# Kernel tuning notes

Hardware: AMD Instinct MI355X
Metric: run time of the kernel (lower is better)

Reference implementation:

```python
import jax, jax.numpy as jnp
import numpy as np

EPS = 1e-8


def _three_nn_interpolate(coords, ref_coords, features):
    # coords: [B, N, 3], ref_coords: [B, M, 3], features: [B, C, M]
    # squared pairwise distances [B, N, M]
    d2 = (
        jnp.sum(coords * coords, axis=-1, keepdims=True)          # [B, N, 1]
        + jnp.sum(ref_coords * ref_coords, axis=-1)[:, None, :]    # [B, 1, M]
        - 2.0 * jnp.einsum('bnd,bmd->bnm', coords, ref_coords)
    )
    neg_d, idx = jax.lax.top_k(-d2, 3)       # 3 nearest -> idx [B, N, 3]
    dist = -neg_d                             # squared dists of 3-NN
    w = 1.0 / (dist + EPS)
    w = w / jnp.sum(w, axis=-1, keepdims=True)  # [B, N, 3]
    feats_t = jnp.swapaxes(features, 1, 2)    # [B, M, C]
    gathered = jax.vmap(lambda f, i: f[i])(feats_t, idx)  # [B, N, 3, C]
    out = jnp.einsum('bnk,bnkc->bcn', w, gathered)         # [B, C, N]
    return out


def setup_inputs() -> dict:
    key = jax.random.key(0)
    ks = jax.random.split(key, 5)
    B, N, M = 2, 16384, 4096
    return {
        'coords': jax.random.normal(ks[0], (B, N, 3), dtype=jnp.float32),
        'ref_coords': jax.random.normal(ks[1], (B, M, 3), dtype=jnp.float32),
        'ref_features': jax.random.normal(ks[2], (B, 256, M), dtype=jnp.float32),
        'ref_t_embed': jax.random.normal(ks[3], (B, 128, M), dtype=jnp.float32),
        'points_features': jax.random.normal(ks[4], (B, 64, N), dtype=jnp.float32),
    }


def reference(coords, ref_coords, ref_features, ref_t_embed, points_features):
    # PointNetFPModule.forward: interpolate features and t_embed from the
    # coarse ref point set onto the dense point set, then concat skip features.
    features = _three_nn_interpolate(coords, ref_coords, ref_features)  # [B, 256, N]
    t_embed = _three_nn_interpolate(coords, ref_coords, ref_t_embed)    # [B, 128, N]
    features = jnp.concatenate([features, points_features], axis=1)     # [B, 320, N]
    return features, t_embed
```

## Files before the change

### kernel.cpp

```cpp
#include <hip/hip_runtime.h>
#include <cstdint>

#define BB 2
#define NN 16384
#define MM 4096
#define CF 256
#define CT 128
#define CP 64

#define TPB1 512
#define NPB1 64
#define CHUNK 2048

__global__ __launch_bounds__(TPB1, 4) void knn_kernel(
    const float* __restrict__ coords,
    const float* __restrict__ ref_coords,
    int4* __restrict__ wsI,
    float4* __restrict__ wsW)
{
#pragma clang fp contract(off)
    __shared__ float4 refs[CHUNK];

    const int tid = threadIdx.x;
    const int b   = blockIdx.y;
    const int n0  = blockIdx.x * NPB1;

    const int pl = tid >> 3;
    const int s  = tid & 7;
    const int n  = n0 + pl;

    const float* cp = coords + ((size_t)b * NN + n) * 3;
    const float cx = cp[0];
    const float cy = cp[1];
    const float cz = cp[2];
    const float cc = (cx * cx + cy * cy) + cz * cz;

    float d0 = INFINITY, d1 = INFINITY, d2v = INFINITY;
    int   i0 = 0, i1 = 0, i2 = 0;
    float tau = INFINITY;
    float thr = INFINITY;

    const float* rc = ref_coords + (size_t)b * MM * 3;

    for (int ch = 0; ch < MM / CHUNK; ++ch) {
        __syncthreads();
        for (int e = tid; e < CHUNK; e += TPB1) {
            const int j = ch * CHUNK + e;
            const float x = rc[3 * j + 0];
            const float y = rc[3 * j + 1];
            const float z = rc[3 * j + 2];
            refs[e] = make_float4(x + x, y + y, z + z, (x * x + y * y) + z * z);
        }
        __syncthreads();

        const int jbase = ch * CHUNK;
        for (int it0 = 0; it0 < CHUNK / 8; it0 += 32) {
            #pragma unroll 4
            for (int k = 0; k < 32; ++k) {
                const int e = s + ((it0 + k) << 3);
                const float4 r = refs[e];
                const float dot2 = (cx * r.x + cy * r.y) + cz * r.z;
                const float dd   = (cc + r.w) - dot2;
                if (__any(dd < thr)) {
                    const int j = jbase + e;
                    const bool l2 = dd < d2v;
                    const bool l1 = dd < d1;
                    const bool l0 = dd < d0;
                    i2 = l2 ? (l1 ? i1 : j) : i2;
                    i1 = l1 ? (l0 ? i0 : j) : i1;
                    i0 = l0 ? j : i0;
                    const float n2  = __builtin_amdgcn_fmed3f(dd, d1, d2v);
                    const float n1  = __builtin_amdgcn_fmed3f(dd, d0, d1);
                    const float nv0 = fminf(dd, d0);
                    d2v = n2; d1 = n1; d0 = nv0;
                    thr = fminf(d2v, tau);
                }
            }
            float t = d2v;
            t = fminf(t, __shfl_xor(t, 1, 64));
            t = fminf(t, __shfl_xor(t, 2, 64));
            t = fminf(t, __shfl_xor(t, 4, 64));
            tau = t;
            thr = fminf(d2v, tau);
        }
    }

    auto ins = [&](float e, int f) {
        const bool l2 = (e < d2v) || (e == d2v && f < i2);
        const bool l1 = (e < d1)  || (e == d1  && f < i1);
        const bool l0 = (e < d0)  || (e == d0  && f < i0);
        d2v = l2 ? (l1 ? d1 : e) : d2v;  i2 = l2 ? (l1 ? i1 : f) : i2;
        d1  = l1 ? (l0 ? d0 : e) : d1;   i1 = l1 ? (l0 ? i0 : f) : i1;
        d0  = l0 ? e : d0;               i0 = l0 ? f : i0;
    };

    for (int off = 1; off < 8; off <<= 1) {
        const float e0 = __shfl_xor(d0,  off, 64);
        const float e1 = __shfl_xor(d1,  off, 64);
        const float e2 = __shfl_xor(d2v, off, 64);
        const int   f0 = __shfl_xor(i0,  off, 64);
        const int   f1 = __shfl_xor(i1,  off, 64);
        const int   f2 = __shfl_xor(i2,  off, 64);
        ins(e0, f0);
        ins(e1, f1);
        ins(e2, f2);
    }

    if (s == 0) {
        float w0 = 1.0f / (d0  + 1e-8f);
        float w1 = 1.0f / (d1  + 1e-8f);
        float w2 = 1.0f / (d2v + 1e-8f);
        const float sum = (w0 + w1) + w2;
        wsI[(size_t)b * NN + n] = make_int4(i0, i1, i2, 0);
        wsW[(size_t)b * NN + n] = make_float4(w0 / sum, w1 / sum, w2 / sum, 0.0f);
    }
}

#define TPB2 256

__global__ __launch_bounds__(TPB2, 8) void interp_kernel(
    const float* __restrict__ refF,
    const float* __restrict__ refT,
    const float* __restrict__ pf,
    const int4*  __restrict__ wsI,
    const float4* __restrict__ wsW,
    float* __restrict__ out)
{
#pragma clang fp contract(off)
    __shared__ float row[MM];
    const int tid  = threadIdx.x;
    const int task = blockIdx.x;
    const size_t outT_base = (size_t)BB * (CF + CP) * NN;

    const float* src;
    float* dst;
    int b;
    if (task < BB * CF) {
        b = task >> 8;
        const int c = task & (CF - 1);
        src = refF + ((size_t)b * CF + c) * MM;
        dst = out + ((size_t)b * (CF + CP) + c) * NN;
    } else if (task < BB * (CF + CT)) {
        const int t2 = task - BB * CF;
        b = t2 >> 7;
        const int c = t2 & (CT - 1);
        src = refT + ((size_t)b * CT + c) * MM;
        dst = out + outT_base + ((size_t)b * CT + c) * NN;
    } else {
        const int t3 = task - BB * (CF + CT);
        const int bb = t3 >> 6;
        const int c  = t3 & (CP - 1);
        const float4* s4 = (const float4*)(pf + ((size_t)bb * CP + c) * NN);
        float4* d4 = (float4*)(out + ((size_t)bb * (CF + CP) + CF + c) * NN);
        for (int i = tid; i < NN / 4; i += TPB2) d4[i] = s4[i];
        return;
    }

    for (int i = tid; i < MM / 4; i += TPB2)
        ((float4*)row)[i] = ((const float4*)src)[i];
    __syncthreads();

    const int4*  wi = wsI + (size_t)b * NN;
    const float4* ww = wsW + (size_t)b * NN;
    for (int nq = tid; nq < NN; nq += TPB2) {
        const int4  id = wi[nq];
        const float4 w = ww[nq];
        dst[nq] = (w.x * row[id.x] + w.y * row[id.y]) + w.z * row[id.z];
    }
}

extern "C" void kernel_launch(void* const* d_in, const int* in_sizes, int n_in,
                              void* d_out, int out_size, void* d_ws, size_t ws_size,
                              hipStream_t stream) {
    const float* coords     = (const float*)d_in[0];
    const float* ref_coords = (const float*)d_in[1];
    const float* refF       = (const float*)d_in[2];
    const float* refT       = (const float*)d_in[3];
    const float* pf         = (const float*)d_in[4];
    float* out = (float*)d_out;

    int4*   wsI = (int4*)d_ws;
    float4* wsW = (float4*)((char*)d_ws + (size_t)BB * NN * sizeof(int4));

    hipLaunchKernelGGL(knn_kernel, dim3(NN / NPB1, BB), dim3(TPB1), 0, stream,
                       coords, ref_coords, wsI, wsW);
    hipLaunchKernelGGL(interp_kernel, dim3(BB * (CF + CT + CP)), dim3(TPB2), 0, stream,
                       refF, refT, pf, wsI, wsW, out);
}
```

Measured before the change: 173.0 us.

## Widen KNN lane split to 16 and interpolate two channels per block

The KNN kernel now splits each query point across 16 lanes instead of 8, using 32 points per block. It also processes two reference candidates per ballot check, which halves the number of __any votes. The interpolation kernel stages two channel rows in shared memory per block, so each index/weight load is reused for two outputs, and it prefetches the next index/weight. The copy blocks each handle four rows. Extra costs are a longer cross-lane merge, index clamping, and doubled LDS use per interp block, which may lower occupancy.

```diff
diff --git a/kernel.cpp b/kernel.cpp
--- a/kernel.cpp
+++ b/kernel.cpp
@@ -9,10 +9,10 @@
 #define CP 64
 
 #define TPB1 512
-#define NPB1 64
+#define NPB1 32
 #define CHUNK 2048
 
-__global__ __launch_bounds__(TPB1, 4) void knn_kernel(
+__global__ __launch_bounds__(TPB1, 8) void knn_kernel(
     const float* __restrict__ coords,
     const float* __restrict__ ref_coords,
     int4* __restrict__ wsI,
@@ -25,8 +25,8 @@
     const int b   = blockIdx.y;
     const int n0  = blockIdx.x * NPB1;
 
-    const int pl = tid >> 3;
-    const int s  = tid & 7;
+    const int pl = tid >> 4;
+    const int s  = tid & 15;
     const int n  = n0 + pl;
 
     const float* cp = coords + ((size_t)b * NN + n) * 3;
@@ -41,6 +41,19 @@
     float thr = INFINITY;
 
     const float* rc = ref_coords + (size_t)b * MM * 3;
+
+    auto upd = [&](float dd, int j) {
+        const bool l2 = dd < d2v;
+        const bool l1 = dd < d1;
+        const bool l0 = dd < d0;
+        i2 = l2 ? (l1 ? i1 : j) : i2;
+        i1 = l1 ? (l0 ? i0 : j) : i1;
+        i0 = l0 ? j : i0;
+        const float n2  = __builtin_amdgcn_fmed3f(dd, d1, d2v);
+        const float n1  = __builtin_amdgcn_fmed3f(dd, d0, d1);
+        const float nv0 = fminf(dd, d0);
+        d2v = n2; d1 = n1; d0 = nv0;
+    };
 
     for (int ch = 0; ch < MM / CHUNK; ++ch) {
         __syncthreads();
@@ -54,33 +67,29 @@
         __syncthreads();
 
         const int jbase = ch * CHUNK;
-        for (int it0 = 0; it0 < CHUNK / 8; it0 += 32) {
-            #pragma unroll 4
-            for (int k = 0; k < 32; ++k) {
-                const int e = s + ((it0 + k) << 3);
-                const float4 r = refs[e];
-                const float dot2 = (cx * r.x + cy * r.y) + cz * r.z;
-                const float dd   = (cc + r.w) - dot2;
-                if (__any(dd < thr)) {
-                    const int j = jbase + e;
-                    const bool l2 = dd < d2v;
-                    const bool l1 = dd < d1;
-                    const bool l0 = dd < d0;
-                    i2 = l2 ? (l1 ? i1 : j) : i2;
-                    i1 = l1 ? (l0 ? i0 : j) : i1;
-                    i0 = l0 ? j : i0;
-                    const float n2  = __builtin_amdgcn_fmed3f(dd, d1, d2v);
-                    const float n1  = __builtin_amdgcn_fmed3f(dd, d0, d1);
-                    const float nv0 = fminf(dd, d0);
-                    d2v = n2; d1 = n1; d0 = nv0;
+        for (int seg = 0; seg < CHUNK / (16 * 32); ++seg) {
+            #pragma unroll
+            for (int t = 0; t < 16; ++t) {
+                const int ea = s + ((seg * 32 + t * 2) << 4);
+                const float4 ra = refs[ea];
+                const float4 rb = refs[ea + 16];
+                const float dot2a = (cx * ra.x + cy * ra.y) + cz * ra.z;
+                const float dda   = (cc + ra.w) - dot2a;
+                const float dot2b = (cx * rb.x + cy * rb.y) + cz * rb.z;
+                const float ddb   = (cc + rb.w) - dot2b;
+                if (__any(fminf(dda, ddb) < thr)) {
+                    const int ja = jbase + ea;
+                    upd(dda, ja);
+                    upd(ddb, ja + 16);
                     thr = fminf(d2v, tau);
                 }
             }
-            float t = d2v;
-            t = fminf(t, __shfl_xor(t, 1, 64));
-            t = fminf(t, __shfl_xor(t, 2, 64));
-            t = fminf(t, __shfl_xor(t, 4, 64));
-            tau = t;
+            float tt = d2v;
+            tt = fminf(tt, __shfl_xor(tt, 1, 64));
+            tt = fminf(tt, __shfl_xor(tt, 2, 64));
+            tt = fminf(tt, __shfl_xor(tt, 4, 64));
+            tt = fminf(tt, __shfl_xor(tt, 8, 64));
+            tau = tt;
             thr = fminf(d2v, tau);
         }
     }
@@ -94,7 +103,7 @@
         d0  = l0 ? e : d0;               i0 = l0 ? f : i0;
     };
 
-    for (int off = 1; off < 8; off <<= 1) {
+    for (int off = 1; off < 16; off <<= 1) {
         const float e0 = __shfl_xor(d0,  off, 64);
         const float e1 = __shfl_xor(d1,  off, 64);
         const float e2 = __shfl_xor(d2v, off, 64);
@@ -116,7 +125,9 @@
     }
 }
 
-#define TPB2 256
+#define TPB2 512
+#define NIB  (BB * (CF + CT) / 2)
+#define NCB  32
 
 __global__ __launch_bounds__(TPB2, 8) void interp_kernel(
     const float* __restrict__ refF,
@@ -127,45 +138,66 @@
     float* __restrict__ out)
 {
 #pragma clang fp contract(off)
-    __shared__ float row[MM];
+    __shared__ float rowA[MM];
+    __shared__ float rowB[MM];
     const int tid  = threadIdx.x;
     const int task = blockIdx.x;
     const size_t outT_base = (size_t)BB * (CF + CP) * NN;
 
-    const float* src;
-    float* dst;
+    if (task >= NIB) {
+        const int t3 = task - NIB;
+        for (int j = 0; j < 4; ++j) {
+            const int r  = t3 * 4 + j;
+            const int bb = r >> 6;
+            const int c  = r & (CP - 1);
+            const float4* s4 = (const float4*)(pf + ((size_t)bb * CP + c) * NN);
+            float4* d4 = (float4*)(out + ((size_t)bb * (CF + CP) + CF + c) * NN);
+            for (int i = tid; i < NN / 4; i += TPB2) d4[i] = s4[i];
+        }
+        return;
+    }
+
+    const int r0 = task * 2;
+    const float* src0;
+    float* dst0;
     int b;
-    if (task < BB * CF) {
-        b = task >> 8;
-        const int c = task & (CF - 1);
-        src = refF + ((size_t)b * CF + c) * MM;
-        dst = out + ((size_t)b * (CF + CP) + c) * NN;
-    } else if (task < BB * (CF + CT)) {
-        const int t2 = task - BB * CF;
-        b = t2 >> 7;
-        const int c = t2 & (CT - 1);
-        src = refT + ((size_t)b * CT + c) * MM;
-        dst = out + outT_base + ((size_t)b * CT + c) * NN;
+    if (r0 < BB * CF) {
+        b = r0 >> 8;
+        const int c = r0 & (CF - 1);
+        src0 = refF + ((size_t)b * CF + c) * MM;
+        dst0 = out + ((size_t)b * (CF + CP) + c) * NN;
     } else {
-        const int t3 = task - BB * (CF + CT);
-        const int bb = t3 >> 6;
-        const int c  = t3 & (CP - 1);
-        const float4* s4 = (const float4*)(pf + ((size_t)bb * CP + c) * NN);
-        float4* d4 = (float4*)(out + ((size_t)bb * (CF + CP) + CF + c) * NN);
-        for (int i = tid; i < NN / 4; i += TPB2) d4[i] = s4[i];
-        return;
-    }
-
-    for (int i = tid; i < MM / 4; i += TPB2)
-        ((float4*)row)[i] = ((const float4*)src)[i];
+        const int r2 = r0 - BB * CF;
+        b = r2 >> 7;
+        const int c = r2 & (CT - 1);
+        src0 = refT + ((size_t)b * CT + c) * MM;
+        dst0 = out + outT_base + ((size_t)b * CT + c) * NN;
+    }
+    const float* src1 = src0 + MM;
+    float* dst1 = dst0 + NN;
+
+    for (int i = tid; i < MM / 4; i += TPB2) {
+        ((float4*)rowA)[i] = ((const float4*)src0)[i];
+        ((float4*)rowB)[i] = ((const float4*)src1)[i];
+    }
     __syncthreads();
 
-    const int4*  wi = wsI + (size_t)b * NN;
+    const int4*   wi = wsI + (size_t)b * NN;
     const float4* ww = wsW + (size_t)b * NN;
+
+    auto clampi = [](int v) { return v < 0 ? 0 : (v > MM - 1 ? MM - 1 : v); };
+
+    int4   id = wi[tid];
+    float4 w  = ww[tid];
     for (int nq = tid; nq < NN; nq += TPB2) {
-        const int4  id = wi[nq];
-        const float4 w = ww[nq];
-        dst[nq] = (w.x * row[id.x] + w.y * row[id.y]) + w.z * row[id.z];
+        const int nq2 = nq + TPB2;
+        int4   idn;
+        float4 wn;
+        if (nq2 < NN) { idn = wi[nq2]; wn = ww[nq2]; }
+        const int a0 = clampi(id.x), a1 = clampi(id.y), a2 = clampi(id.z);
+        dst0[nq] = (w.x * rowA[a0] + w.y * rowA[a1]) + w.z * rowA[a2];
+        dst1[nq] = (w.x * rowB[a0] + w.y * rowB[a1]) + w.z * rowB[a2];
+        id = idn; w = wn;
     }
 }
 
@@ -184,6 +216,6 @@
 
     hipLaunchKernelGGL(knn_kernel, dim3(NN / NPB1, BB), dim3(TPB1), 0, stream,
                        coords, ref_coords, wsI, wsW);
-    hipLaunchKernelGGL(interp_kernel, dim3(BB * (CF + CT + CP)), dim3(TPB2), 0, stream,
+    hipLaunchKernelGGL(interp_kernel, dim3(NIB + NCB), dim3(TPB2), 0, stream,
                        refF, refT, pf, wsI, wsW, out);
 }
```

Result: no change. 173.9 us (+0.6%).
